# Kernel optimization log

Hardware: AMD Instinct MI355X
Metric: run time of the kernel (lower is better)

Reference implementation:

```python
import jax, jax.numpy as jnp
import numpy as np

H = W = 224
NUM_COLS = 1024          # static padded ring width (>= max pixels in any radial ring, ~703)
SHUFFLE_FRACTION = 0.5
BATCH = 128

def _build_maps():
    centre = (H // 2, W // 2)
    Y, X = np.ogrid[:H, :W]
    dist = np.round(np.sqrt((X - centre[0]) ** 2 + (Y - centre[1]) ** 2)).astype(np.int32)
    num_rows = int(dist[0, 0]) + 1
    ax2 = np.zeros_like(dist)
    for d in range(num_rows):
        m = dist == d
        ax2[m] = np.arange(m.sum(), dtype=np.int32)  # row-major order within each ring
    return dist, ax2, num_rows

_DIST_NP, _AX2_NP, NUM_ROWS = _build_maps()
DIST_FLAT = jnp.asarray(_DIST_NP.reshape(-1))  # (H*W,) radial bin of each pixel
AX2_FLAT = jnp.asarray(_AX2_NP.reshape(-1))    # (H*W,) index within its ring

def _process_one(img, mrand, prand):
    # img: (H, W); mrand: (H, W); prand: (NUM_ROWS, NUM_COLS)
    sel = mrand < SHUFFLE_FRACTION
    masked = jnp.where(sel, img, jnp.nan)
    # scatter selected pixels into polar bins (pixel -> (dist, ax2) is a bijection)
    polar = jnp.full((NUM_ROWS, NUM_COLS), jnp.nan, dtype=img.dtype)
    polar = polar.at[DIST_FLAT, AX2_FLAT].set(masked.reshape(-1))
    # random per-row permutation of columns
    perm = jnp.argsort(prand, axis=1)
    shuf = jnp.take_along_axis(polar, perm, axis=1)
    # compact the non-NaN shuffled values (in column order) back into the
    # originally-occupied columns (in ascending order) -- same as the TF
    # argsort(dists)/boolean-mask scatter, expressed with static shapes.
    src_order = jnp.argsort(jnp.isnan(shuf), axis=1)    # stable: non-NaN cols first
    vals = jnp.take_along_axis(shuf, src_order, axis=1)
    dst_order = jnp.argsort(jnp.isnan(polar), axis=1)   # stable: occupied cols first
    rows = jnp.arange(NUM_ROWS)[:, None]
    reinserted = shuf.at[rows, dst_order].set(vals)
    # gather each pixel's (possibly shuffled) value and write back selected pixels
    new_vals = reinserted[DIST_FLAT, AX2_FLAT].reshape(H, W)
    return jnp.where(sel, new_vals, img)

def setup_inputs() -> dict:
    key = jax.random.key(0)
    k1, k2, k3 = jax.random.split(key, 3)
    images = jax.random.normal(k1, (BATCH, H, W, 1), dtype=jnp.float32)
    mask_rand = jax.random.uniform(k2, (BATCH, H, W), dtype=jnp.float32)
    perm_rand = jax.random.uniform(k3, (BATCH, NUM_ROWS, NUM_COLS), dtype=jnp.float32)
    return {"images": images, "mask_rand": mask_rand, "perm_rand": perm_rand}

def reference(images, mask_rand, perm_rand):
    out = jax.vmap(_process_one)(images[..., 0], mask_rand, perm_rand)
    return out[..., None]
```

## Files before the change

kernel.cpp:

```cpp
#include <hip/hip_runtime.h>

#define IMG_H 224
#define IMG_W 224
#define HW (IMG_H * IMG_W)
#define HWB (HW / 8)
#define NUM_ROWS 159
#define NUM_COLS 1024
#define BATCH 128
#define OVF_CAP 4096
#define MAXC 12
#define NBUCK 512
#define NHWORDS (NBUCK / 2)
#define WPL (NHWORDS / 64)

__device__ __forceinline__ int isqrt_i(int v) {
    int u = (int)sqrtf((float)v);
    while (u > 0 && u * u > v) --u;
    while ((u + 1) * (u + 1) <= v) ++u;
    return u;
}

__device__ __forceinline__ void lds_fence() {
    asm volatile("s_waitcnt lgkmcnt(0)" ::: "memory");
}

__global__ __launch_bounds__(256) void pre_pass(
    const float4* __restrict__ img4, const float4* __restrict__ mask4,
    float4* __restrict__ out4, unsigned char* __restrict__ selb,
    unsigned short* __restrict__ ring_pix, int* __restrict__ ring_cnt,
    int* __restrict__ ovf_cnt) {
    const int bid = blockIdx.x;
    const int tid = threadIdx.x;
    __shared__ int scnt[256];

    if (bid < NUM_ROWS) {
        const int d = bid;
        if (d == 0 && tid == 0) ovf_cnt[0] = 0;
        int cnt = 0;
        int x0l = 0, x1l = -1, x0r = 0, x1r = -1;
        if (tid < IMG_H) {
            const int dy = tid - 112;
            const int Araw = (d == 0) ? 0 : (d * d - d + 1);
            int A = Araw - dy * dy;
            if (A < 0) A = 0;
            const int B = d * d + d - dy * dy;
            if (B >= 0) {
                const int hi = isqrt_i(B);
                int lo = isqrt_i(A);
                if (lo * lo < A) ++lo;
                if (lo <= hi) {
                    if (lo == 0) {
                        x0l = 112 - min(hi, 112);
                        x1l = 112 + min(hi, 111);
                    } else {
                        x0l = 112 - min(hi, 112);
                        x1l = 112 - lo;
                        x0r = 112 + lo;
                        x1r = 112 + min(hi, 111);
                    }
                    cnt = max(0, x1l - x0l + 1) + max(0, x1r - x0r + 1);
                }
            }
        }
        scnt[tid] = cnt;
        __syncthreads();
        for (int off = 1; off < 256; off <<= 1) {
            const int mine = scnt[tid];
            const int add = (tid >= off) ? scnt[tid - off] : 0;
            __syncthreads();
            scnt[tid] = mine + add;
            __syncthreads();
        }
        if (tid < IMG_H && cnt > 0) {
            int j = d * NUM_COLS + (scnt[tid] - cnt);
            const int rowbase = tid * IMG_W;
            for (int x = x0l; x <= x1l; ++x) ring_pix[j++] = (unsigned short)(rowbase + x);
            for (int x = x0r; x <= x1r; ++x) ring_pix[j++] = (unsigned short)(rowbase + x);
        }
        if (tid == 255) ring_cnt[d] = scnt[255];
    } else {
        const int t = (bid - NUM_ROWS) * 256 + tid;
        const float4 i0 = img4[2 * t];
        const float4 i1 = img4[2 * t + 1];
        const float4 m0 = mask4[2 * t];
        const float4 m1 = mask4[2 * t + 1];
        out4[2 * t] = i0;
        out4[2 * t + 1] = i1;
        const unsigned by = (m0.x < 0.5f ? 1u : 0u) | (m0.y < 0.5f ? 2u : 0u) |
                            (m0.z < 0.5f ? 4u : 0u) | (m0.w < 0.5f ? 8u : 0u) |
                            (m1.x < 0.5f ? 16u : 0u) | (m1.y < 0.5f ? 32u : 0u) |
                            (m1.z < 0.5f ? 64u : 0u) | (m1.w < 0.5f ? 128u : 0u);
        selb[t] = (unsigned char)by;
    }
}

__device__ __forceinline__ void sort_run2(unsigned* __restrict__ k32,
                                          unsigned short* __restrict__ j16,
                                          int s, int e) {
    for (int i = s + 1; i < e; ++i) {
        const unsigned key = k32[i];
        const unsigned short jj = j16[i];
        int q = i - 1;
        while (q >= s && (k32[q] > key || (k32[q] == key && j16[q] > jj))) {
            k32[q + 1] = k32[q];
            j16[q + 1] = j16[q];
            --q;
        }
        k32[q + 1] = key;
        j16[q + 1] = jj;
    }
}

template <int CAP>
__device__ int gather_count_sort(
    int b, int d, int lane, int n,
    const float* __restrict__ img, const unsigned char* __restrict__ selb,
    const float* __restrict__ prand, float* __restrict__ out,
    const unsigned short* __restrict__ ring_pix,
    unsigned* __restrict__ srt32, unsigned short* __restrict__ srtj,
    unsigned* __restrict__ hist, float* __restrict__ vlds) {
    const float* imgb = img + (size_t)b * HW;
    const unsigned char* sbb = selb + (size_t)b * HWB;
    const float* prb = prand + ((size_t)b * NUM_ROWS + d) * NUM_COLS;
    float* outb = out + (size_t)b * HW;
    const unsigned long long ltmask = (1ull << lane) - 1ull;
    const unsigned short* rp = ring_pix + d * NUM_COLS;

#pragma unroll
    for (int t = 0; t < WPL; ++t) hist[t * 64 + lane] = 0;

    int p[MAXC];
    unsigned char sb[MAXC];
    unsigned kb[MAXC];
#pragma unroll
    for (int c = 0; c < MAXC; ++c)
        if (c * 64 < n) p[c] = rp[min(c * 64 + lane, n - 1)];
#pragma unroll
    for (int c = 0; c < MAXC; ++c)
        if (c * 64 < n) sb[c] = sbb[p[c] >> 3];
#pragma unroll
    for (int c = 0; c < MAXC; ++c)
        if (c * 64 < n) kb[c] = __float_as_uint(prb[c * 64 + lane]);

    unsigned selm = 0;
#pragma unroll
    for (int c = 0; c < MAXC; ++c)
        if (c * 64 < n) {
            if ((c * 64 + lane) < n && ((sb[c] >> (p[c] & 7)) & 1)) selm |= 1u << c;
        }

    float v[MAXC];
#pragma unroll
    for (int c = 0; c < MAXC; ++c)
        if (c * 64 < n) {
            if ((selm >> c) & 1) v[c] = imgb[p[c]];
        }

    lds_fence();

    int jc[MAXC];
    int base = 0;
#pragma unroll
    for (int c = 0; c < MAXC; ++c)
        if (c * 64 < n) {
            const bool sel = (selm >> c) & 1;
            const unsigned long long ball = __ballot(sel);
            if (sel) {
                jc[c] = base + __popcll(ball & ltmask);
                const int bk = (int)(__uint_as_float(kb[c]) * (float)NBUCK);
                atomicAdd(&hist[bk >> 1], 1u << ((bk & 1) * 16));
            }
            base += __popcll(ball);
        }
    const int base_static = base;
    for (int c0 = MAXC * 64; c0 < n; c0 += 64) {
        const int i = c0 + lane;
        bool sel = false;
        int pp = 0;
        unsigned kk = 0;
        if (i < n) {
            pp = rp[i];
            kk = __float_as_uint(prb[i]);
            sel = (sbb[pp >> 3] >> (pp & 7)) & 1;
        }
        const unsigned long long ball = __ballot(sel);
        if (sel) {
            const int j = base + __popcll(ball & ltmask);
            if (j < CAP) vlds[j] = imgb[pp];
            const int bk = (int)(__uint_as_float(kk) * (float)NBUCK);
            atomicAdd(&hist[bk >> 1], 1u << ((bk & 1) * 16));
        }
        base += __popcll(ball);
    }
    const int k = base;
    if (k > CAP) return k;
    if (k == 0) return 0;

    lds_fence();

    unsigned neww[WPL];
    unsigned run = 0;
#pragma unroll
    for (int t = 0; t < WPL; ++t) {
        const unsigned w = hist[lane * WPL + t];
        const unsigned c0 = w & 0xffffu;
        neww[t] = run | ((run + c0) << 16);
        run += c0 + (w >> 16);
    }
    const unsigned own = run;
#pragma unroll
    for (int off = 1; off < 64; off <<= 1) {
        const unsigned o = __shfl_up(run, off, 64);
        if (lane >= off) run += o;
    }
    const unsigned bx = run - own;
    const unsigned bxp = bx | (bx << 16);
    unsigned st[WPL];
#pragma unroll
    for (int t = 0; t < WPL; ++t) {
        st[t] = neww[t] + bxp;
        hist[lane * WPL + t] = st[t];
    }

    lds_fence();

#pragma unroll
    for (int c = 0; c < MAXC; ++c)
        if (c * 64 < n) {
            if ((selm >> c) & 1) {
                const int bk = (int)(__uint_as_float(kb[c]) * (float)NBUCK);
                const unsigned sh = (unsigned)((bk & 1) * 16);
                const unsigned old = atomicAdd(&hist[bk >> 1], 1u << sh);
                const int pos = (int)((old >> sh) & 0xffffu);
                srt32[pos] = kb[c];
                srtj[pos] = (unsigned short)jc[c];
                vlds[jc[c]] = v[c];
            }
        }
    int tb = base_static;
    for (int c0 = MAXC * 64; c0 < n; c0 += 64) {
        const int i = c0 + lane;
        bool sel = false;
        int pp = 0;
        unsigned kk = 0;
        if (i < n) {
            pp = rp[i];
            kk = __float_as_uint(prb[i]);
            sel = (sbb[pp >> 3] >> (pp & 7)) & 1;
        }
        const unsigned long long ball = __ballot(sel);
        if (sel) {
            const int j = tb + __popcll(ball & ltmask);
            const int bk = (int)(__uint_as_float(kk) * (float)NBUCK);
            const unsigned sh = (unsigned)((bk & 1) * 16);
            const unsigned old = atomicAdd(&hist[bk >> 1], 1u << sh);
            const int pos = (int)((old >> sh) & 0xffffu);
            srt32[pos] = kk;
            srtj[pos] = (unsigned short)j;
        }
        tb += __popcll(ball);
    }

    lds_fence();

#pragma unroll
    for (int t = 0; t < WPL; ++t) {
        const unsigned wend = hist[lane * WPL + t];
        const unsigned ws0 = st[t];
        sort_run2(srt32, srtj, (int)(ws0 & 0xffffu), (int)(wend & 0xffffu));
        sort_run2(srt32, srtj, (int)(ws0 >> 16), (int)(wend >> 16));
    }

    lds_fence();

#pragma unroll
    for (int c = 0; c < MAXC; ++c)
        if (c * 64 < n) {
            if ((selm >> c) & 1) {
                const int jp = srtj[jc[c]];
                outb[p[c]] = vlds[jp];
            }
        }
    tb = base_static;
    for (int c0 = MAXC * 64; c0 < n; c0 += 64) {
        const int i = c0 + lane;
        bool sel = false;
        int pp = 0;
        if (i < n) {
            pp = rp[i];
            sel = (sbb[pp >> 3] >> (pp & 7)) & 1;
        }
        const unsigned long long ball = __ballot(sel);
        if (sel) {
            const int j = tb + __popcll(ball & ltmask);
            const int jp = srtj[j];
            outb[pp] = vlds[jp];
        }
        tb += __popcll(ball);
    }
    return k;
}

__global__ __launch_bounds__(256, 6) void radial_shuffle(
    const float* __restrict__ img, const unsigned char* __restrict__ selb,
    const float* __restrict__ prand, float* __restrict__ out,
    const unsigned short* __restrict__ ring_pix, const int* __restrict__ ring_cnt,
    int* __restrict__ ovf_cnt, int* __restrict__ ovf_list) {
    const int tid = threadIdx.x;
    const int wid = tid >> 6;
    const int lane = tid & 63;
    const int xcd = blockIdx.x & 7;
    const int g = (blockIdx.x >> 3) * 4 + wid;
    const int b = xcd * (BATCH / 8) + g / NUM_ROWS;
    const int d = g % NUM_ROWS;
    const int n = __builtin_amdgcn_readfirstlane(ring_cnt[d]);

    __shared__ unsigned srt32_s[4][512];
    __shared__ unsigned short srtj_s[4][512];
    __shared__ unsigned hist_s[4][NHWORDS];
    __shared__ float vl_s[4][512];

    const int k = gather_count_sort<512>(b, d, lane, n, img, selb, prand, out,
                                         ring_pix, srt32_s[wid], srtj_s[wid],
                                         hist_s[wid], vl_s[wid]);

    if (k > 512) {
        if (lane == 0) {
            const int idx = atomicAdd(ovf_cnt, 1);
            if (idx < OVF_CAP) ovf_list[idx] = b * NUM_ROWS + d;
        }
    }
}

__global__ __launch_bounds__(64) void overflow_sort(
    const float* __restrict__ img, const unsigned char* __restrict__ selb,
    const float* __restrict__ prand, float* __restrict__ out,
    const unsigned short* __restrict__ ring_pix, const int* __restrict__ ring_cnt,
    const int* __restrict__ ovf_cnt, const int* __restrict__ ovf_list) {
    __shared__ unsigned srt32[1024];
    __shared__ unsigned short srtj[1024];
    __shared__ unsigned hist[NHWORDS];
    __shared__ float vlds[1024];
    const int m = min(*ovf_cnt, OVF_CAP);
    const int lane = threadIdx.x;
    for (int t = blockIdx.x; t < m; t += gridDim.x) {
        const int bd = ovf_list[t];
        const int b = bd / NUM_ROWS;
        const int d = bd % NUM_ROWS;
        const int n = __builtin_amdgcn_readfirstlane(ring_cnt[d]);
        gather_count_sort<1024>(b, d, lane, n, img, selb, prand, out, ring_pix,
                                srt32, srtj, hist, vlds);
        __syncthreads();
    }
}

extern "C" void kernel_launch(void* const* d_in, const int* in_sizes, int n_in,
                              void* d_out, int out_size, void* d_ws, size_t ws_size,
                              hipStream_t stream) {
    const float* img   = (const float*)d_in[0];
    const float* mask  = (const float*)d_in[1];
    const float* prand = (const float*)d_in[2];
    float* out = (float*)d_out;

    unsigned short* ring_pix = (unsigned short*)d_ws;
    int* ring_cnt = (int*)((char*)d_ws + NUM_ROWS * NUM_COLS * sizeof(unsigned short));
    int* ovf_cnt  = ring_cnt + NUM_ROWS;
    int* ovf_list = ovf_cnt + 1;
    unsigned char* selb = (unsigned char*)(ovf_list + OVF_CAP);

    hipLaunchKernelGGL(pre_pass, dim3(NUM_ROWS + BATCH * HW / 8 / 256), dim3(256),
                       0, stream, (const float4*)img, (const float4*)mask,
                       (float4*)out, selb, ring_pix, ring_cnt, ovf_cnt);
    hipLaunchKernelGGL(radial_shuffle, dim3(BATCH * NUM_ROWS / 4), dim3(256), 0,
                       stream, img, selb, prand, out, ring_pix, ring_cnt,
                       ovf_cnt, ovf_list);
    hipLaunchKernelGGL(overflow_sort, dim3(32), dim3(64), 0, stream,
                       img, selb, prand, out, ring_pix, ring_cnt,
                       ovf_cnt, ovf_list);
}
```

Before: 198.4 us.

## Pack sort key and index into 64-bit entries and split static/dynamic ring paths

Sort entries now pack the random key and the source index into a single 64-bit LDS word, so the insertion sort compares and moves one value instead of two arrays. The static path takes each element's bucket offset from the first histogram atomic and adds it to the scanned bucket start, which removes the second atomic pass. It also skips the bucket sort entirely when no bucket holds two or more entries. Rings wider than MAXC*64 go to a separate non-unrolled dynamic function. MAXC, the occupancy hint and the overflow grid size are all lowered, which trades register pressure against waves per CU.

```diff
diff --git a/kernel.cpp b/kernel.cpp
--- a/kernel.cpp
+++ b/kernel.cpp
@@ -8,7 +8,7 @@
 #define NUM_COLS 1024
 #define BATCH 128
 #define OVF_CAP 4096
-#define MAXC 12
+#define MAXC 11
 #define NBUCK 512
 #define NHWORDS (NBUCK / 2)
 #define WPL (NHWORDS / 64)
@@ -94,20 +94,16 @@
     }
 }
 
-__device__ __forceinline__ void sort_run2(unsigned* __restrict__ k32,
-                                          unsigned short* __restrict__ j16,
-                                          int s, int e) {
+__device__ __forceinline__ void sort_run(unsigned long long* __restrict__ srt,
+                                         int s, int e) {
     for (int i = s + 1; i < e; ++i) {
-        const unsigned key = k32[i];
-        const unsigned short jj = j16[i];
+        const unsigned long long key = srt[i];
         int q = i - 1;
-        while (q >= s && (k32[q] > key || (k32[q] == key && j16[q] > jj))) {
-            k32[q + 1] = k32[q];
-            j16[q + 1] = j16[q];
+        while (q >= s && srt[q] > key) {
+            srt[q + 1] = srt[q];
             --q;
         }
-        k32[q + 1] = key;
-        j16[q + 1] = jj;
+        srt[q + 1] = key;
     }
 }
 
@@ -117,8 +113,8 @@
     const float* __restrict__ img, const unsigned char* __restrict__ selb,
     const float* __restrict__ prand, float* __restrict__ out,
     const unsigned short* __restrict__ ring_pix,
-    unsigned* __restrict__ srt32, unsigned short* __restrict__ srtj,
-    unsigned* __restrict__ hist, float* __restrict__ vlds) {
+    unsigned long long* __restrict__ srt, unsigned* __restrict__ hist,
+    float* __restrict__ vlds) {
     const float* imgb = img + (size_t)b * HW;
     const unsigned char* sbb = selb + (size_t)b * HWB;
     const float* prb = prand + ((size_t)b * NUM_ROWS + d) * NUM_COLS;
@@ -158,7 +154,7 @@
 
     lds_fence();
 
-    int jc[MAXC];
+    int jc[MAXC], oldc[MAXC];
     int base = 0;
 #pragma unroll
     for (int c = 0; c < MAXC; ++c)
@@ -168,19 +164,112 @@
             if (sel) {
                 jc[c] = base + __popcll(ball & ltmask);
                 const int bk = (int)(__uint_as_float(kb[c]) * (float)NBUCK);
-                atomicAdd(&hist[bk >> 1], 1u << ((bk & 1) * 16));
+                const unsigned sh = (unsigned)((bk & 1) * 16);
+                const unsigned old = atomicAdd(&hist[bk >> 1], 1u << sh);
+                oldc[c] = (int)((old >> sh) & 0xffffu);
             }
             base += __popcll(ball);
         }
-    const int base_static = base;
-    for (int c0 = MAXC * 64; c0 < n; c0 += 64) {
+    const int k = base;
+    if (k > CAP) return k;
+    if (k == 0) return 0;
+
+    lds_fence();
+
+    unsigned cw[WPL], stw[WPL];
+    unsigned run = 0;
+#pragma unroll
+    for (int t = 0; t < WPL; ++t) {
+        const unsigned w = hist[lane * WPL + t];
+        cw[t] = w;
+        const unsigned c0 = w & 0xffffu;
+        stw[t] = run | ((run + c0) << 16);
+        run += c0 + (w >> 16);
+    }
+    const unsigned own = run;
+#pragma unroll
+    for (int off = 1; off < 64; off <<= 1) {
+        const unsigned o = __shfl_up(run, off, 64);
+        if (lane >= off) run += o;
+    }
+    const unsigned bx = run - own;
+    const unsigned bxp = bx | (bx << 16);
+#pragma unroll
+    for (int t = 0; t < WPL; ++t) {
+        stw[t] += bxp;
+        hist[lane * WPL + t] = stw[t];
+    }
+
+    lds_fence();
+
+#pragma unroll
+    for (int c = 0; c < MAXC; ++c)
+        if (c * 64 < n) {
+            if ((selm >> c) & 1) {
+                const int bk = (int)(__uint_as_float(kb[c]) * (float)NBUCK);
+                const unsigned sh = (unsigned)((bk & 1) * 16);
+                const int pos = (int)((hist[bk >> 1] >> sh) & 0xffffu) + oldc[c];
+                srt[pos] = ((unsigned long long)kb[c] << 16) | (unsigned)jc[c];
+                vlds[jc[c]] = v[c];
+            }
+        }
+
+    lds_fence();
+
+    bool any2 = false;
+#pragma unroll
+    for (int t = 0; t < WPL; ++t)
+        if ((cw[t] & 0xffffu) >= 2 || (cw[t] >> 16) >= 2) any2 = true;
+    if (__ballot(any2) != 0ull) {
+#pragma unroll
+        for (int t = 0; t < WPL; ++t) {
+            const unsigned s0 = stw[t] & 0xffffu, c0 = cw[t] & 0xffffu;
+            const unsigned s1 = stw[t] >> 16, c1 = cw[t] >> 16;
+            if (c0 >= 2) sort_run(srt, (int)s0, (int)(s0 + c0));
+            if (c1 >= 2) sort_run(srt, (int)s1, (int)(s1 + c1));
+        }
+        lds_fence();
+    }
+
+    const unsigned short* s16 = (const unsigned short*)srt;
+#pragma unroll
+    for (int c = 0; c < MAXC; ++c)
+        if (c * 64 < n) {
+            if ((selm >> c) & 1) {
+                const int jp = s16[4 * jc[c]];
+                outb[p[c]] = vlds[jp];
+            }
+        }
+    return k;
+}
+
+template <int CAP>
+__device__ int gather_count_sort_dyn(
+    int b, int d, int lane, int n,
+    const float* __restrict__ img, const unsigned char* __restrict__ selb,
+    const float* __restrict__ prand, float* __restrict__ out,
+    const unsigned short* __restrict__ ring_pix,
+    unsigned long long* __restrict__ srt, unsigned* __restrict__ hist,
+    float* __restrict__ vlds) {
+    const float* imgb = img + (size_t)b * HW;
+    const unsigned char* sbb = selb + (size_t)b * HWB;
+    const float* prb = prand + ((size_t)b * NUM_ROWS + d) * NUM_COLS;
+    float* outb = out + (size_t)b * HW;
+    const unsigned long long ltmask = (1ull << lane) - 1ull;
+    const unsigned short* rp = ring_pix + d * NUM_COLS;
+
+    for (int t = 0; t < WPL; ++t) hist[t * 64 + lane] = 0;
+    lds_fence();
+
+    int base = 0;
+    for (int c0 = 0; c0 < n; c0 += 64) {
         const int i = c0 + lane;
         bool sel = false;
         int pp = 0;
         unsigned kk = 0;
         if (i < n) {
             pp = rp[i];
-            kk = __float_as_uint(prb[i]);
+            kk = __float_as_uint(prb[min(i, NUM_COLS - 1)]);
             sel = (sbb[pp >> 3] >> (pp & 7)) & 1;
         }
         const unsigned long long ball = __ballot(sel);
@@ -195,12 +284,10 @@
     const int k = base;
     if (k > CAP) return k;
     if (k == 0) return 0;
-
     lds_fence();
 
     unsigned neww[WPL];
     unsigned run = 0;
-#pragma unroll
     for (int t = 0; t < WPL; ++t) {
         const unsigned w = hist[lane * WPL + t];
         const unsigned c0 = w & 0xffffu;
@@ -208,7 +295,6 @@
         run += c0 + (w >> 16);
     }
     const unsigned own = run;
-#pragma unroll
     for (int off = 1; off < 64; off <<= 1) {
         const unsigned o = __shfl_up(run, off, 64);
         if (lane >= off) run += o;
@@ -216,73 +302,46 @@
     const unsigned bx = run - own;
     const unsigned bxp = bx | (bx << 16);
     unsigned st[WPL];
-#pragma unroll
     for (int t = 0; t < WPL; ++t) {
         st[t] = neww[t] + bxp;
         hist[lane * WPL + t] = st[t];
     }
-
-    lds_fence();
-
-#pragma unroll
-    for (int c = 0; c < MAXC; ++c)
-        if (c * 64 < n) {
-            if ((selm >> c) & 1) {
-                const int bk = (int)(__uint_as_float(kb[c]) * (float)NBUCK);
-                const unsigned sh = (unsigned)((bk & 1) * 16);
-                const unsigned old = atomicAdd(&hist[bk >> 1], 1u << sh);
-                const int pos = (int)((old >> sh) & 0xffffu);
-                srt32[pos] = kb[c];
-                srtj[pos] = (unsigned short)jc[c];
-                vlds[jc[c]] = v[c];
-            }
-        }
-    int tb = base_static;
-    for (int c0 = MAXC * 64; c0 < n; c0 += 64) {
+    lds_fence();
+
+    int jb = 0;
+    for (int c0 = 0; c0 < n; c0 += 64) {
         const int i = c0 + lane;
         bool sel = false;
-        int pp = 0;
         unsigned kk = 0;
         if (i < n) {
-            pp = rp[i];
-            kk = __float_as_uint(prb[i]);
+            const int pp = rp[i];
+            kk = __float_as_uint(prb[min(i, NUM_COLS - 1)]);
             sel = (sbb[pp >> 3] >> (pp & 7)) & 1;
         }
         const unsigned long long ball = __ballot(sel);
         if (sel) {
-            const int j = tb + __popcll(ball & ltmask);
+            const int j = jb + __popcll(ball & ltmask);
             const int bk = (int)(__uint_as_float(kk) * (float)NBUCK);
             const unsigned sh = (unsigned)((bk & 1) * 16);
             const unsigned old = atomicAdd(&hist[bk >> 1], 1u << sh);
             const int pos = (int)((old >> sh) & 0xffffu);
-            srt32[pos] = kk;
-            srtj[pos] = (unsigned short)j;
-        }
-        tb += __popcll(ball);
-    }
-
-    lds_fence();
-
-#pragma unroll
+            srt[pos] = ((unsigned long long)kk << 16) | (unsigned)j;
+        }
+        jb += __popcll(ball);
+    }
+    lds_fence();
+
     for (int t = 0; t < WPL; ++t) {
         const unsigned wend = hist[lane * WPL + t];
         const unsigned ws0 = st[t];
-        sort_run2(srt32, srtj, (int)(ws0 & 0xffffu), (int)(wend & 0xffffu));
-        sort_run2(srt32, srtj, (int)(ws0 >> 16), (int)(wend >> 16));
-    }
-
-    lds_fence();
-
-#pragma unroll
-    for (int c = 0; c < MAXC; ++c)
-        if (c * 64 < n) {
-            if ((selm >> c) & 1) {
-                const int jp = srtj[jc[c]];
-                outb[p[c]] = vlds[jp];
-            }
-        }
-    tb = base_static;
-    for (int c0 = MAXC * 64; c0 < n; c0 += 64) {
+        sort_run(srt, (int)(ws0 & 0xffffu), (int)(wend & 0xffffu));
+        sort_run(srt, (int)(ws0 >> 16), (int)(wend >> 16));
+    }
+    lds_fence();
+
+    const unsigned short* s16 = (const unsigned short*)srt;
+    jb = 0;
+    for (int c0 = 0; c0 < n; c0 += 64) {
         const int i = c0 + lane;
         bool sel = false;
         int pp = 0;
@@ -292,16 +351,16 @@
         }
         const unsigned long long ball = __ballot(sel);
         if (sel) {
-            const int j = tb + __popcll(ball & ltmask);
-            const int jp = srtj[j];
+            const int j = jb + __popcll(ball & ltmask);
+            const int jp = s16[4 * j];
             outb[pp] = vlds[jp];
         }
-        tb += __popcll(ball);
+        jb += __popcll(ball);
     }
     return k;
 }
 
-__global__ __launch_bounds__(256, 6) void radial_shuffle(
+__global__ __launch_bounds__(256, 5) void radial_shuffle(
     const float* __restrict__ img, const unsigned char* __restrict__ selb,
     const float* __restrict__ prand, float* __restrict__ out,
     const unsigned short* __restrict__ ring_pix, const int* __restrict__ ring_cnt,
@@ -315,14 +374,19 @@
     const int d = g % NUM_ROWS;
     const int n = __builtin_amdgcn_readfirstlane(ring_cnt[d]);
 
-    __shared__ unsigned srt32_s[4][512];
-    __shared__ unsigned short srtj_s[4][512];
+    __shared__ unsigned long long srt_s[4][512];
     __shared__ unsigned hist_s[4][NHWORDS];
     __shared__ float vl_s[4][512];
 
-    const int k = gather_count_sort<512>(b, d, lane, n, img, selb, prand, out,
-                                         ring_pix, srt32_s[wid], srtj_s[wid],
-                                         hist_s[wid], vl_s[wid]);
+    int k;
+    if (n <= MAXC * 64) {
+        k = gather_count_sort<512>(b, d, lane, n, img, selb, prand, out,
+                                   ring_pix, srt_s[wid], hist_s[wid], vl_s[wid]);
+    } else {
+        k = gather_count_sort_dyn<512>(b, d, lane, n, img, selb, prand, out,
+                                       ring_pix, srt_s[wid], hist_s[wid],
+                                       vl_s[wid]);
+    }
 
     if (k > 512) {
         if (lane == 0) {
@@ -337,8 +401,7 @@
     const float* __restrict__ prand, float* __restrict__ out,
     const unsigned short* __restrict__ ring_pix, const int* __restrict__ ring_cnt,
     const int* __restrict__ ovf_cnt, const int* __restrict__ ovf_list) {
-    __shared__ unsigned srt32[1024];
-    __shared__ unsigned short srtj[1024];
+    __shared__ unsigned long long srt[1024];
     __shared__ unsigned hist[NHWORDS];
     __shared__ float vlds[1024];
     const int m = min(*ovf_cnt, OVF_CAP);
@@ -348,8 +411,13 @@
         const int b = bd / NUM_ROWS;
         const int d = bd % NUM_ROWS;
         const int n = __builtin_amdgcn_readfirstlane(ring_cnt[d]);
-        gather_count_sort<1024>(b, d, lane, n, img, selb, prand, out, ring_pix,
-                                srt32, srtj, hist, vlds);
+        if (n <= MAXC * 64) {
+            gather_count_sort<1024>(b, d, lane, n, img, selb, prand, out,
+                                    ring_pix, srt, hist, vlds);
+        } else {
+            gather_count_sort_dyn<1024>(b, d, lane, n, img, selb, prand, out,
+                                        ring_pix, srt, hist, vlds);
+        }
         __syncthreads();
     }
 }
@@ -374,7 +442,7 @@
     hipLaunchKernelGGL(radial_shuffle, dim3(BATCH * NUM_ROWS / 4), dim3(256), 0,
                        stream, img, selb, prand, out, ring_pix, ring_cnt,
                        ovf_cnt, ovf_list);
-    hipLaunchKernelGGL(overflow_sort, dim3(32), dim3(64), 0, stream,
+    hipLaunchKernelGGL(overflow_sort, dim3(16), dim3(64), 0, stream,
                        img, selb, prand, out, ring_pix, ring_cnt,
                        ovf_cnt, ovf_list);
 }
```

Result: slower. 206.8 us (+4.2%).
